# Performance work log

Measured on AMD Instinct MI355X. Metric: run time of the kernel, lower is better.

## Reference

```python
import jax, jax.numpy as jnp
import numpy as np

H = 1024
BUDGET = 4096
R = BUDGET // 2          # recurrent_size
L = BUDGET - R           # local branch size
B, S = 4, 2048


def setup_inputs() -> dict:
    key = jax.random.key(0)
    ks = jax.random.split(key, 10)
    sc_h = 1.0 / np.sqrt(H)
    sc_r = 1.0 / np.sqrt(R)
    sc_l = 1.0 / np.sqrt(L)
    return {
        "x": jax.random.normal(ks[0], (B, S, H), dtype=jnp.float32),
        "W_forget": jax.random.normal(ks[1], (R, H), dtype=jnp.float32) * sc_h,
        "W_input": jax.random.normal(ks[2], (R, H), dtype=jnp.float32) * sc_h,
        "W_value": jax.random.normal(ks[3], (R, H), dtype=jnp.float32) * sc_h,
        "W_query": jax.random.normal(ks[4], (R, H), dtype=jnp.float32) * sc_h,
        "W_rec_out": jax.random.normal(ks[5], (H, R), dtype=jnp.float32) * sc_r,
        "W_up": jax.random.normal(ks[6], (L, H), dtype=jnp.float32) * sc_h,
        "W_gate": jax.random.normal(ks[7], (L, H), dtype=jnp.float32) * sc_h,
        "W_down": jax.random.normal(ks[8], (H, L), dtype=jnp.float32) * sc_l,
        "initial_state": jnp.zeros((R,), dtype=jnp.float32),
    }


def reference(x, W_forget, W_input, W_value, W_query, W_rec_out,
              W_up, W_gate, W_down, initial_state):
    # Batch all token projections once (torch Linear: y = x @ W.T).
    f = jnp.tanh(jnp.einsum("bsh,rh->bsr", x, W_forget))          # [B,S,R]
    g = jax.nn.sigmoid(jnp.einsum("bsh,rh->bsr", x, W_input))     # write gate
    c = jax.nn.silu(jnp.einsum("bsh,rh->bsr", x, W_value))        # candidate
    q = jnp.einsum("bsh,rh->bsr", x, W_query)

    # Diagonal linear recurrence: state_t = f_t * state_{t-1} + g_t * c_t
    state0 = jnp.broadcast_to(initial_state[None, :], (x.shape[0], initial_state.shape[0]))

    def step(state, fgc):
        f_t, gc_t = fgc
        new_state = f_t * state + gc_t
        return new_state, new_state

    # time-major xs for scan
    _, states = jax.lax.scan(step, state0,
                             (jnp.swapaxes(f, 0, 1), jnp.swapaxes(g * c, 0, 1)))
    states = jnp.swapaxes(states, 0, 1)                            # [B,S,R]

    readout = jax.nn.silu(q * states)                              # [B,S,R]
    rec = jnp.einsum("bsr,hr->bsh", readout, W_rec_out)

    # SwiGLU local branch (dropout = 0 / eval mode)
    up = jnp.einsum("bsh,lh->bsl", x, W_up)
    gate = jax.nn.silu(jnp.einsum("bsh,lh->bsl", x, W_gate))
    local = jnp.einsum("bsl,hl->bsh", up * gate, W_down)

    return rec + local                                             # [B,S,H]
```

## Files before the change

### kernel.cpp

```cpp
#include <hip/hip_runtime.h>
#include <hip/hip_bf16.h>

typedef __attribute__((ext_vector_type(8))) short bf16x8;
typedef __attribute__((ext_vector_type(4))) float f32x4;

#define DEV __device__ __forceinline__

DEV float fsigmoid(float x){ return 1.0f/(1.0f + __expf(-x)); }
DEV float fsilu(float x){ return x/(1.0f + __expf(-x)); }
DEV float ftanh(float x){ return 1.0f - 2.0f/(1.0f + __expf(2.0f*x)); }

DEV unsigned short f2bf(float x){
  __hip_bfloat16 h = __float2bfloat16(x);
  return *reinterpret_cast<unsigned short*>(&h);
}
DEV float bf2f(unsigned short u){ return __uint_as_float(((unsigned)u) << 16); }

typedef const __attribute__((address_space(1))) unsigned int* gas_ptr;
typedef __attribute__((address_space(3))) unsigned int* las_ptr;
DEV void gload16(const void* gp, void* lp){
  __builtin_amdgcn_global_load_lds((gas_ptr)gp, (las_ptr)lp, 16, 0, 0);
}


__global__ __launch_bounds__(256) void k_conv_x(const float* __restrict__ src, __hip_bfloat16* __restrict__ dst){
  size_t gid = (size_t)blockIdx.x*256 + threadIdx.x;
  size_t base = gid*8;
  f32x4 a = *(const f32x4*)(src+base);
  f32x4 b = *(const f32x4*)(src+base+4);
  bf16x8 o;
#pragma unroll
  for(int j=0;j<4;j++){ o[j]=(short)f2bf(a[j]); o[4+j]=(short)f2bf(b[j]); }
  *(bf16x8*)((unsigned short*)dst + base) = o;
}

__global__ __launch_bounds__(256) void k_conv_w1(const float* __restrict__ Wf,const float* __restrict__ Wq,
    const float* __restrict__ Wi,const float* __restrict__ Wv,const float* __restrict__ Wu,
    const float* __restrict__ Wg, __hip_bfloat16* __restrict__ W1){
  int gid = blockIdx.x*256 + threadIdx.x;
  int row = gid>>7; int col = (gid&127)*8;
  int seg = row>>11; int sr = row & 2047;
  const float* s;
  if(seg==0)s=Wf; else if(seg==1)s=Wq; else if(seg==2)s=Wi; else if(seg==3)s=Wv; else if(seg==4)s=Wu; else s=Wg;
  const float* p = s + (size_t)sr*1024 + col;
  f32x4 a = *(const f32x4*)p; f32x4 b = *(const f32x4*)(p+4);
  bf16x8 o;
#pragma unroll
  for(int j=0;j<4;j++){ o[j]=(short)f2bf(a[j]); o[4+j]=(short)f2bf(b[j]); }
  *(bf16x8*)((unsigned short*)W1 + (size_t)row*1024 + col) = o;
}

__global__ __launch_bounds__(256) void k_conv_w2(const float* __restrict__ Wro, const float* __restrict__ Wd,
    __hip_bfloat16* __restrict__ W2){
  int gid = blockIdx.x*256 + threadIdx.x;
  int row = gid>>9; int col = (gid&511)*8;
  const float* p = (col<2048) ? (Wro + (size_t)row*2048 + col) : (Wd + (size_t)row*2048 + (col-2048));
  f32x4 a = *(const f32x4*)p; f32x4 b = *(const f32x4*)(p+4);
  bf16x8 o;
#pragma unroll
  for(int j=0;j<4;j++){ o[j]=(short)f2bf(a[j]); o[4+j]=(short)f2bf(b[j]); }
  *(bf16x8*)((unsigned short*)W2 + (size_t)row*4096 + col) = o;
}


__global__ __launch_bounds__(256) void k_gemm1(const __hip_bfloat16* __restrict__ A, const __hip_bfloat16* __restrict__ B,
    float* __restrict__ fb, float* __restrict__ gb, float* __restrict__ cb,
    __hip_bfloat16* __restrict__ qb, __hip_bfloat16* __restrict__ upg){
  const int K = 1024;
  __shared__ __hip_bfloat16 sA[128*32];
  __shared__ __hip_bfloat16 sB[128*32];
  int bid = blockIdx.x;
  int cpx = gridDim.x >> 3;
  bid = (bid & 7)*cpx + (bid >> 3);
  int bm = bid/96, bn = bid%96;
  int t = threadIdx.x, w = t>>6, lane = t&63;
  int wr = w>>1, wc = w&1;

  f32x4 zero = {0.f,0.f,0.f,0.f};
  f32x4 acc[4][4];
#pragma unroll
  for(int i=0;i<4;i++)
#pragma unroll
    for(int j=0;j<4;j++) acc[i][j] = zero;

  const int frow = lane&15;
  const int kofs = (lane>>4)*8;
  const unsigned short* Ag = (const unsigned short*)A;
  const unsigned short* Bg = (const unsigned short*)B;

  for(int kt=0; kt<K; kt+=32){
#pragma unroll
    for(int i=0;i<2;i++){
      int c = i*256 + t;
      gload16(Ag + (size_t)(bm*128 + (c>>2))*K + kt + (c&3)*8, (char*)sA + (i*256 + w*64)*16);
      gload16(Bg + (size_t)(bn*128 + (c>>2))*K + kt + (c&3)*8, (char*)sB + (i*256 + w*64)*16);
    }
    __syncthreads();
    bf16x8 af[4], bfr[4];
#pragma unroll
    for(int mi=0;mi<4;mi++) af[mi]  = *(const bf16x8*)&sA[(wr*64 + mi*16 + frow)*32 + kofs];
#pragma unroll
    for(int ni=0;ni<4;ni++) bfr[ni] = *(const bf16x8*)&sB[(wc*64 + ni*16 + frow)*32 + kofs];
#pragma unroll
    for(int mi=0;mi<4;mi++)
#pragma unroll
      for(int ni=0;ni<4;ni++)
        acc[mi][ni] = __builtin_amdgcn_mfma_f32_16x16x32_bf16(af[mi], bfr[ni], acc[mi][ni], 0,0,0);
    __syncthreads();
  }

  int seg = bn/16;
  int row0 = bm*128 + wr*64 + ((lane>>4)<<2);
  int colL = ((bn*128)&2047) + wc*64 + (lane&15);

#define EPI(STMT) \
  _Pragma("unroll") for(int mi=0;mi<4;mi++) \
  _Pragma("unroll") for(int ni=0;ni<4;ni++) \
  _Pragma("unroll") for(int j=0;j<4;j++) { \
    int rr=row0+mi*16+j; int cc=colL+ni*16; float v=acc[mi][ni][j]; STMT; }

  if(seg==0)      { EPI( fb[(size_t)rr*2048+cc] = ftanh(v) ) }
  else if(seg==1) { EPI( qb[(size_t)rr*2048+cc] = __float2bfloat16(v) ) }
  else if(seg==2) { EPI( gb[(size_t)rr*2048+cc] = fsigmoid(v) ) }
  else if(seg==3) { EPI( cb[(size_t)rr*2048+cc] = fsilu(v) ) }
  else if(seg==4) { EPI( upg[(size_t)rr*4096+cc] = __float2bfloat16(v) ) }
  else            { EPI( upg[(size_t)rr*4096+2048+cc] = __float2bfloat16(fsilu(v)) ) }
#undef EPI
}

#define NC 64
#define CHL 32

__global__ __launch_bounds__(256) void k_scanA(const float* __restrict__ f_, const float* __restrict__ g_,
    const float* __restrict__ c_, float* __restrict__ Fp_, float* __restrict__ Sl_){
  int blk = blockIdx.x; int b = blk>>6; int ch = blk&63;
  int r0 = threadIdx.x*8;
  float st[8], Fp[8];
#pragma unroll
  for(int j=0;j<8;j++){ st[j]=0.f; Fp[j]=1.f; }
  size_t base = ((size_t)(b*2048 + ch*CHL))*2048 + r0;
#pragma unroll 4
  for(int s=0;s<CHL;s++){
    size_t o = base + (size_t)s*2048;
    float fv[8], gv[8], cv[8];
    *(f32x4*)&fv[0]=*(const f32x4*)(f_+o); *(f32x4*)&fv[4]=*(const f32x4*)(f_+o+4);
    *(f32x4*)&gv[0]=*(const f32x4*)(g_+o); *(f32x4*)&gv[4]=*(const f32x4*)(g_+o+4);
    *(f32x4*)&cv[0]=*(const f32x4*)(c_+o); *(f32x4*)&cv[4]=*(const f32x4*)(c_+o+4);
#pragma unroll
    for(int j=0;j<8;j++){ st[j] = fv[j]*st[j] + gv[j]*cv[j]; Fp[j] *= fv[j]; }
  }
  size_t so = ((size_t)blk)*2048 + r0;
  *(f32x4*)(Fp_+so)   = *(f32x4*)&Fp[0]; *(f32x4*)(Fp_+so+4) = *(f32x4*)&Fp[4];
  *(f32x4*)(Sl_+so)   = *(f32x4*)&st[0]; *(f32x4*)(Sl_+so+4) = *(f32x4*)&st[4];
}

__global__ __launch_bounds__(256) void k_scanB(const float* __restrict__ Fp_, const float* __restrict__ Sl_,
    const float* __restrict__ init, float* __restrict__ Cin_){
  int gid = blockIdx.x*256 + threadIdx.x;
  int b = gid>>11; int r = gid&2047;
  float carry = init[r];
  for(int ch=0; ch<NC; ch++){
    size_t o = ((size_t)(b*NC+ch))*2048 + r;
    Cin_[o] = carry;
    carry = Fp_[o]*carry + Sl_[o];
  }
}

__global__ __launch_bounds__(256) void k_scanC(const float* __restrict__ f_, const float* __restrict__ g_,
    const float* __restrict__ c_, unsigned short* qro, const float* __restrict__ Cin_){
  int blk = blockIdx.x; int b = blk>>6; int ch = blk&63;
  int r0 = threadIdx.x*8;
  float st[8];
  size_t so = ((size_t)blk)*2048 + r0;
  *(f32x4*)&st[0] = *(const f32x4*)(Cin_+so);
  *(f32x4*)&st[4] = *(const f32x4*)(Cin_+so+4);
  size_t base = ((size_t)(b*2048 + ch*CHL))*2048 + r0;
#pragma unroll 2
  for(int s=0;s<CHL;s++){
    size_t o = base + (size_t)s*2048;
    float fv[8], gv[8], cv[8];
    *(f32x4*)&fv[0]=*(const f32x4*)(f_+o); *(f32x4*)&fv[4]=*(const f32x4*)(f_+o+4);
    *(f32x4*)&gv[0]=*(const f32x4*)(g_+o); *(f32x4*)&gv[4]=*(const f32x4*)(g_+o+4);
    *(f32x4*)&cv[0]=*(const f32x4*)(c_+o); *(f32x4*)&cv[4]=*(const f32x4*)(c_+o+4);
    bf16x8 qu = *(const bf16x8*)(qro + o);
    bf16x8 ov;
#pragma unroll
    for(int j=0;j<8;j++){
      st[j] = fv[j]*st[j] + gv[j]*cv[j];
      float qv = bf2f((unsigned short)qu[j]);
      ov[j] = (short)f2bf(fsilu(qv*st[j]));
    }
    *(bf16x8*)(qro + o) = ov;
  }
}

__global__ __launch_bounds__(256) void k_ew_ug(__hip_bfloat16* __restrict__ upg){
  size_t gid = (size_t)blockIdx.x*256 + threadIdx.x;
  size_t m = gid>>8; size_t l0 = (gid&255)*8;
  unsigned short* p = (unsigned short*)upg;
  bf16x8 uv = *(const bf16x8*)(p + m*4096 + l0);
  bf16x8 gv = *(const bf16x8*)(p + m*4096 + 2048 + l0);
  bf16x8 ov;
#pragma unroll
  for(int j=0;j<8;j++){
    float u = bf2f((unsigned short)uv[j]);
    float g = bf2f((unsigned short)gv[j]);
    ov[j] = (short)f2bf(u*g);
  }
  *(bf16x8*)(p + m*4096 + l0) = ov;
}

__global__ __launch_bounds__(256) void k_gemm2(const __hip_bfloat16* __restrict__ RO, const __hip_bfloat16* __restrict__ UPG,
    const __hip_bfloat16* __restrict__ B, float* __restrict__ out){
  __shared__ __hip_bfloat16 sA[128*32];
  __shared__ __hip_bfloat16 sB[128*32];
  int bid = blockIdx.x;
  int cpx = gridDim.x >> 3;
  bid = (bid & 7)*cpx + (bid >> 3);
  int bm = bid>>3, bn = bid&7;
  int t = threadIdx.x, w = t>>6, lane = t&63;
  int wr = w>>1, wc = w&1;

  f32x4 zero = {0.f,0.f,0.f,0.f};
  f32x4 acc[4][4];
#pragma unroll
  for(int i=0;i<4;i++)
#pragma unroll
    for(int j=0;j<4;j++) acc[i][j] = zero;

  const int frow = lane&15;
  const int kofs = (lane>>4)*8;
  const unsigned short* ROg  = (const unsigned short*)RO;
  const unsigned short* UPGg = (const unsigned short*)UPG;
  const unsigned short* Bg   = (const unsigned short*)B;

  for(int kt=0; kt<4096; kt+=32){
    const unsigned short* Abase; size_t ld; int kk;
    if(kt < 2048){ Abase = ROg;  ld = 2048; kk = kt; }
    else         { Abase = UPGg; ld = 4096; kk = kt - 2048; }
#pragma unroll
    for(int i=0;i<2;i++){
      int c = i*256 + t;
      gload16(Abase + (size_t)(bm*128 + (c>>2))*ld + kk + (c&3)*8, (char*)sA + (i*256 + w*64)*16);
      gload16(Bg + (size_t)(bn*128 + (c>>2))*4096 + kt + (c&3)*8, (char*)sB + (i*256 + w*64)*16);
    }
    __syncthreads();
    bf16x8 af[4], bfr[4];
#pragma unroll
    for(int mi=0;mi<4;mi++) af[mi]  = *(const bf16x8*)&sA[(wr*64 + mi*16 + frow)*32 + kofs];
#pragma unroll
    for(int ni=0;ni<4;ni++) bfr[ni] = *(const bf16x8*)&sB[(wc*64 + ni*16 + frow)*32 + kofs];
#pragma unroll
    for(int mi=0;mi<4;mi++)
#pragma unroll
      for(int ni=0;ni<4;ni++)
        acc[mi][ni] = __builtin_amdgcn_mfma_f32_16x16x32_bf16(af[mi], bfr[ni], acc[mi][ni], 0,0,0);
    __syncthreads();
  }

  int row0 = bm*128 + wr*64 + ((lane>>4)<<2);
  int col0 = bn*128 + wc*64 + (lane&15);
#pragma unroll
  for(int mi=0;mi<4;mi++)
#pragma unroll
    for(int ni=0;ni<4;ni++)
#pragma unroll
      for(int j=0;j<4;j++)
        out[(size_t)(row0+mi*16+j)*1024 + col0 + ni*16] = acc[mi][ni][j];
}

extern "C" void kernel_launch(void* const* d_in, const int* in_sizes, int n_in,
                              void* d_out, int out_size, void* d_ws, size_t ws_size,
                              hipStream_t stream) {
  (void)in_sizes; (void)n_in; (void)out_size;
  const float* x   = (const float*)d_in[0];
  const float* Wf  = (const float*)d_in[1];
  const float* Wi  = (const float*)d_in[2];
  const float* Wv  = (const float*)d_in[3];
  const float* Wq  = (const float*)d_in[4];
  const float* Wro = (const float*)d_in[5];
  const float* Wu  = (const float*)d_in[6];
  const float* Wg  = (const float*)d_in[7];
  const float* Wd  = (const float*)d_in[8];
  const float* ist = (const float*)d_in[9];
  float* out = (float*)d_out;

  char* w = (char*)d_ws;
  auto alloc = [&](size_t bytes){ char* p = w; w += (bytes + 255) & ~(size_t)255; return p; };

  __hip_bfloat16* xb = (__hip_bfloat16*)alloc(16777216);
  __hip_bfloat16* W1 = (__hip_bfloat16*)alloc(25165824);
  __hip_bfloat16* W2 = (__hip_bfloat16*)alloc(8388608);

  size_t fixed = (size_t)16777216 + 25165824 + 8388608 + 3*256;
  auto need = [&](int CBq)->size_t{
    return fixed + (size_t)CBq*(3*(size_t)16777216 + 8388608 + 16777216 + 3*524288)
                 + 6*256 + (size_t)(1<<20);
  };
  int CB = (ws_size >= need(4)) ? 4 : (ws_size >= need(2)) ? 2 : 1;

  float* fb = (float*)alloc((size_t)CB*16777216);
  float* gb = (float*)alloc((size_t)CB*16777216);
  float* cb = (float*)alloc((size_t)CB*16777216);
  unsigned short* qro = (unsigned short*)alloc((size_t)CB*8388608);
  __hip_bfloat16* upg = (__hip_bfloat16*)alloc((size_t)CB*16777216);
  float* Fp = (float*)alloc((size_t)CB*524288);
  float* Sl = (float*)alloc((size_t)CB*524288);
  float* Ci = (float*)alloc((size_t)CB*524288);

  k_conv_x <<<4096, 256, 0, stream>>>(x, xb);
  k_conv_w1<<<6144, 256, 0, stream>>>(Wf, Wq, Wi, Wv, Wu, Wg, W1);
  k_conv_w2<<<2048, 256, 0, stream>>>(Wro, Wd, W2);

  for(int b0 = 0; b0 < 4; b0 += CB){
    k_gemm1<<<CB*16*96, 256, 0, stream>>>(xb + (size_t)b0*2048*1024, W1, fb, gb, cb,
                                          (__hip_bfloat16*)qro, upg);
    k_scanA<<<CB*64,   256, 0, stream>>>(fb, gb, cb, Fp, Sl);
    k_scanB<<<CB*8,    256, 0, stream>>>(Fp, Sl, ist, Ci);
    k_scanC<<<CB*64,   256, 0, stream>>>(fb, gb, cb, qro, Ci);
    k_ew_ug<<<CB*2048, 256, 0, stream>>>(upg);
    k_gemm2<<<CB*16*8, 256, 0, stream>>>((const __hip_bfloat16*)qro, upg, W2,
                                         out + (size_t)b0*2048*1024);
  }
}
```

Baseline: 722.6 us.

## Store gate and candidate in bf16, retile gemm2 to 64-row tiles, group block swizzle

The gate and candidate activations written by the first GEMM are now stored as bf16 instead of fp32, which halves their write traffic and the read traffic in both scan passes. The forget gate stays fp32 because it compounds along the recurrence. The second GEMM moves from 128x128 to 64x128 tiles, doubling the block count for better occupancy across CUs at the cost of more B-operand reloads. Both GEMMs also get grouped block-index swizzling for better L2 reuse. The bf16 storage adds small precision loss in g*c.

```diff
diff --git a/kernel.cpp b/kernel.cpp
--- a/kernel.cpp
+++ b/kernel.cpp
@@ -64,15 +64,19 @@
 
 
 __global__ __launch_bounds__(256) void k_gemm1(const __hip_bfloat16* __restrict__ A, const __hip_bfloat16* __restrict__ B,
-    float* __restrict__ fb, float* __restrict__ gb, float* __restrict__ cb,
+    float* __restrict__ fb, __hip_bfloat16* __restrict__ gb, __hip_bfloat16* __restrict__ cb,
     __hip_bfloat16* __restrict__ qb, __hip_bfloat16* __restrict__ upg){
   const int K = 1024;
   __shared__ __hip_bfloat16 sA[128*32];
   __shared__ __hip_bfloat16 sB[128*32];
-  int bid = blockIdx.x;
-  int cpx = gridDim.x >> 3;
-  bid = (bid & 7)*cpx + (bid >> 3);
-  int bm = bid/96, bn = bid%96;
+  const int NBN = 96;
+  int raw = blockIdx.x;
+  int per = gridDim.x >> 3;
+  int p = (raw & 7)*per + (raw >> 3);
+  int group = p / (8*NBN);
+  int rem   = p % (8*NBN);
+  int bm = group*8 + (rem & 7);
+  int bn = rem >> 3;
   int t = threadIdx.x, w = t>>6, lane = t&63;
   int wr = w>>1, wc = w&1;
 
@@ -121,8 +125,8 @@
 
   if(seg==0)      { EPI( fb[(size_t)rr*2048+cc] = ftanh(v) ) }
   else if(seg==1) { EPI( qb[(size_t)rr*2048+cc] = __float2bfloat16(v) ) }
-  else if(seg==2) { EPI( gb[(size_t)rr*2048+cc] = fsigmoid(v) ) }
-  else if(seg==3) { EPI( cb[(size_t)rr*2048+cc] = fsilu(v) ) }
+  else if(seg==2) { EPI( gb[(size_t)rr*2048+cc] = __float2bfloat16(fsigmoid(v)) ) }
+  else if(seg==3) { EPI( cb[(size_t)rr*2048+cc] = __float2bfloat16(fsilu(v)) ) }
   else if(seg==4) { EPI( upg[(size_t)rr*4096+cc] = __float2bfloat16(v) ) }
   else            { EPI( upg[(size_t)rr*4096+2048+cc] = __float2bfloat16(fsilu(v)) ) }
 #undef EPI
@@ -131,8 +135,8 @@
 #define NC 64
 #define CHL 32
 
-__global__ __launch_bounds__(256) void k_scanA(const float* __restrict__ f_, const float* __restrict__ g_,
-    const float* __restrict__ c_, float* __restrict__ Fp_, float* __restrict__ Sl_){
+__global__ __launch_bounds__(256) void k_scanA(const float* __restrict__ f_, const unsigned short* __restrict__ g_,
+    const unsigned short* __restrict__ c_, float* __restrict__ Fp_, float* __restrict__ Sl_){
   int blk = blockIdx.x; int b = blk>>6; int ch = blk&63;
   int r0 = threadIdx.x*8;
   float st[8], Fp[8];
@@ -142,12 +146,15 @@
 #pragma unroll 4
   for(int s=0;s<CHL;s++){
     size_t o = base + (size_t)s*2048;
-    float fv[8], gv[8], cv[8];
+    float fv[8];
     *(f32x4*)&fv[0]=*(const f32x4*)(f_+o); *(f32x4*)&fv[4]=*(const f32x4*)(f_+o+4);
-    *(f32x4*)&gv[0]=*(const f32x4*)(g_+o); *(f32x4*)&gv[4]=*(const f32x4*)(g_+o+4);
-    *(f32x4*)&cv[0]=*(const f32x4*)(c_+o); *(f32x4*)&cv[4]=*(const f32x4*)(c_+o+4);
-#pragma unroll
-    for(int j=0;j<8;j++){ st[j] = fv[j]*st[j] + gv[j]*cv[j]; Fp[j] *= fv[j]; }
+    bf16x8 gv8 = *(const bf16x8*)(g_+o);
+    bf16x8 cv8 = *(const bf16x8*)(c_+o);
+#pragma unroll
+    for(int j=0;j<8;j++){
+      float gc = bf2f((unsigned short)gv8[j]) * bf2f((unsigned short)cv8[j]);
+      st[j] = fv[j]*st[j] + gc; Fp[j] *= fv[j];
+    }
   }
   size_t so = ((size_t)blk)*2048 + r0;
   *(f32x4*)(Fp_+so)   = *(f32x4*)&Fp[0]; *(f32x4*)(Fp_+so+4) = *(f32x4*)&Fp[4];
@@ -166,8 +173,8 @@
   }
 }
 
-__global__ __launch_bounds__(256) void k_scanC(const float* __restrict__ f_, const float* __restrict__ g_,
-    const float* __restrict__ c_, unsigned short* qro, const float* __restrict__ Cin_){
+__global__ __launch_bounds__(256) void k_scanC(const float* __restrict__ f_, const unsigned short* __restrict__ g_,
+    const unsigned short* __restrict__ c_, unsigned short* qro, const float* __restrict__ Cin_){
   int blk = blockIdx.x; int b = blk>>6; int ch = blk&63;
   int r0 = threadIdx.x*8;
   float st[8];
@@ -178,15 +185,16 @@
 #pragma unroll 2
   for(int s=0;s<CHL;s++){
     size_t o = base + (size_t)s*2048;
-    float fv[8], gv[8], cv[8];
+    float fv[8];
     *(f32x4*)&fv[0]=*(const f32x4*)(f_+o); *(f32x4*)&fv[4]=*(const f32x4*)(f_+o+4);
-    *(f32x4*)&gv[0]=*(const f32x4*)(g_+o); *(f32x4*)&gv[4]=*(const f32x4*)(g_+o+4);
-    *(f32x4*)&cv[0]=*(const f32x4*)(c_+o); *(f32x4*)&cv[4]=*(const f32x4*)(c_+o+4);
+    bf16x8 gv8 = *(const bf16x8*)(g_+o);
+    bf16x8 cv8 = *(const bf16x8*)(c_+o);
     bf16x8 qu = *(const bf16x8*)(qro + o);
     bf16x8 ov;
 #pragma unroll
     for(int j=0;j<8;j++){
-      st[j] = fv[j]*st[j] + gv[j]*cv[j];
+      float gc = bf2f((unsigned short)gv8[j]) * bf2f((unsigned short)cv8[j]);
+      st[j] = fv[j]*st[j] + gc;
       float qv = bf2f((unsigned short)qu[j]);
       ov[j] = (short)f2bf(fsilu(qv*st[j]));
     }
@@ -210,21 +218,25 @@
   *(bf16x8*)(p + m*4096 + l0) = ov;
 }
 
+
 __global__ __launch_bounds__(256) void k_gemm2(const __hip_bfloat16* __restrict__ RO, const __hip_bfloat16* __restrict__ UPG,
     const __hip_bfloat16* __restrict__ B, float* __restrict__ out){
-  __shared__ __hip_bfloat16 sA[128*32];
+  __shared__ __hip_bfloat16 sA[64*32];
   __shared__ __hip_bfloat16 sB[128*32];
-  int bid = blockIdx.x;
-  int cpx = gridDim.x >> 3;
-  bid = (bid & 7)*cpx + (bid >> 3);
-  int bm = bid>>3, bn = bid&7;
+  int raw = blockIdx.x;
+  int per = gridDim.x >> 3;
+  int p = (raw & 7)*per + (raw >> 3);
+  int group = p >> 6;
+  int rem = p & 63;
+  int bm = group*8 + (rem & 7);
+  int bn = rem >> 3;
   int t = threadIdx.x, w = t>>6, lane = t&63;
   int wr = w>>1, wc = w&1;
 
   f32x4 zero = {0.f,0.f,0.f,0.f};
-  f32x4 acc[4][4];
-#pragma unroll
-  for(int i=0;i<4;i++)
+  f32x4 acc[2][4];
+#pragma unroll
+  for(int i=0;i<2;i++)
 #pragma unroll
     for(int j=0;j<4;j++) acc[i][j] = zero;
 
@@ -238,30 +250,30 @@
     const unsigned short* Abase; size_t ld; int kk;
     if(kt < 2048){ Abase = ROg;  ld = 2048; kk = kt; }
     else         { Abase = UPGg; ld = 4096; kk = kt - 2048; }
+    gload16(Abase + (size_t)(bm*64 + (t>>2))*ld + kk + (t&3)*8, (char*)sA + (w*64)*16);
 #pragma unroll
     for(int i=0;i<2;i++){
       int c = i*256 + t;
-      gload16(Abase + (size_t)(bm*128 + (c>>2))*ld + kk + (c&3)*8, (char*)sA + (i*256 + w*64)*16);
       gload16(Bg + (size_t)(bn*128 + (c>>2))*4096 + kt + (c&3)*8, (char*)sB + (i*256 + w*64)*16);
     }
     __syncthreads();
-    bf16x8 af[4], bfr[4];
-#pragma unroll
-    for(int mi=0;mi<4;mi++) af[mi]  = *(const bf16x8*)&sA[(wr*64 + mi*16 + frow)*32 + kofs];
+    bf16x8 af[2], bfr[4];
+#pragma unroll
+    for(int mi=0;mi<2;mi++) af[mi]  = *(const bf16x8*)&sA[(wr*32 + mi*16 + frow)*32 + kofs];
 #pragma unroll
     for(int ni=0;ni<4;ni++) bfr[ni] = *(const bf16x8*)&sB[(wc*64 + ni*16 + frow)*32 + kofs];
 #pragma unroll
-    for(int mi=0;mi<4;mi++)
+    for(int mi=0;mi<2;mi++)
 #pragma unroll
       for(int ni=0;ni<4;ni++)
         acc[mi][ni] = __builtin_amdgcn_mfma_f32_16x16x32_bf16(af[mi], bfr[ni], acc[mi][ni], 0,0,0);
     __syncthreads();
   }
 
-  int row0 = bm*128 + wr*64 + ((lane>>4)<<2);
+  int row0 = bm*64 + wr*32 + ((lane>>4)<<2);
   int col0 = bn*128 + wc*64 + (lane&15);
 #pragma unroll
-  for(int mi=0;mi<4;mi++)
+  for(int mi=0;mi<2;mi++)
 #pragma unroll
     for(int ni=0;ni<4;ni++)
 #pragma unroll
@@ -294,16 +306,16 @@
 
   size_t fixed = (size_t)16777216 + 25165824 + 8388608 + 3*256;
   auto need = [&](int CBq)->size_t{
-    return fixed + (size_t)CBq*(3*(size_t)16777216 + 8388608 + 16777216 + 3*524288)
-                 + 6*256 + (size_t)(1<<20);
+    return fixed + (size_t)CBq*((size_t)16777216 + 3*8388608 + 16777216 + 3*524288)
+                 + 8*256 + (size_t)(1<<20);
   };
   int CB = (ws_size >= need(4)) ? 4 : (ws_size >= need(2)) ? 2 : 1;
 
-  float* fb = (float*)alloc((size_t)CB*16777216);
-  float* gb = (float*)alloc((size_t)CB*16777216);
-  float* cb = (float*)alloc((size_t)CB*16777216);
-  unsigned short* qro = (unsigned short*)alloc((size_t)CB*8388608);
-  __hip_bfloat16* upg = (__hip_bfloat16*)alloc((size_t)CB*16777216);
+  float* fb          = (float*)alloc((size_t)CB*16777216);
+  unsigned short* gb = (unsigned short*)alloc((size_t)CB*8388608);
+  unsigned short* cb = (unsigned short*)alloc((size_t)CB*8388608);
+  unsigned short* qro= (unsigned short*)alloc((size_t)CB*8388608);
+  __hip_bfloat16* upg= (__hip_bfloat16*)alloc((size_t)CB*16777216);
   float* Fp = (float*)alloc((size_t)CB*524288);
   float* Sl = (float*)alloc((size_t)CB*524288);
   float* Ci = (float*)alloc((size_t)CB*524288);
@@ -313,13 +325,14 @@
   k_conv_w2<<<2048, 256, 0, stream>>>(Wro, Wd, W2);
 
   for(int b0 = 0; b0 < 4; b0 += CB){
-    k_gemm1<<<CB*16*96, 256, 0, stream>>>(xb + (size_t)b0*2048*1024, W1, fb, gb, cb,
+    k_gemm1<<<CB*16*96, 256, 0, stream>>>(xb + (size_t)b0*2048*1024, W1, fb,
+                                          (__hip_bfloat16*)gb, (__hip_bfloat16*)cb,
                                           (__hip_bfloat16*)qro, upg);
     k_scanA<<<CB*64,   256, 0, stream>>>(fb, gb, cb, Fp, Sl);
     k_scanB<<<CB*8,    256, 0, stream>>>(Fp, Sl, ist, Ci);
     k_scanC<<<CB*64,   256, 0, stream>>>(fb, gb, cb, qro, Ci);
     k_ew_ug<<<CB*2048, 256, 0, stream>>>(upg);
-    k_gemm2<<<CB*16*8, 256, 0, stream>>>((const __hip_bfloat16*)qro, upg, W2,
+    k_gemm2<<<CB*32*8, 256, 0, stream>>>((const __hip_bfloat16*)qro, upg, W2,
                                          out + (size_t)b0*2048*1024);
   }
 }
```

New measurement: 655.4 us. 9.3% less time.
